# Performance work log

Measured on AMD Instinct MI355X. Metric: run time of the kernel, lower is better.

The kernel has to match this reference:

```python
import jax, jax.numpy as jnp
import numpy as np

B, D, K = 4096, 768, 60


def setup_inputs() -> dict:
    key = jax.random.key(0)
    k1, k2, k3 = jax.random.split(key, 3)
    user_emb = jax.random.normal(k1, (B, D), dtype=jnp.float32)
    pos_item_emb = jax.random.normal(k2, (B, D), dtype=jnp.float32)
    # Per-row negative indices into the in-batch item table, excluding the
    # row's own positive (emulates the exclusion/sampling done on host in torch).
    r = jax.random.randint(k3, (B, K), 0, B, dtype=jnp.int32)
    rows = jnp.arange(B, dtype=jnp.int32)[:, None]
    neg_indices = jnp.where(r == rows, (r + 1) % B, r)
    return {"user_emb": user_emb, "pos_item_emb": pos_item_emb,
            "neg_indices": neg_indices}


def reference(user_emb, pos_item_emb, neg_indices):
    # u2i contrastive loss: logits = [u.pos, u.neg_1..neg_K], label 0, mean CE.
    logits_pos = jnp.sum(user_emb * pos_item_emb, axis=-1)          # (B,)
    neg_embs = pos_item_emb[neg_indices]                            # (B, K, D)
    logits_neg = jnp.einsum('bd,bkd->bk', user_emb, neg_embs)      # (B, K)
    logits = jnp.concatenate([logits_pos[:, None], logits_neg], axis=1)
    loss = -jax.nn.log_softmax(logits, axis=-1)[:, 0]               # label = 0
    return jnp.mean(loss)
```

## Files before the change

kernel.cpp:

```cpp
#include <hip/hip_runtime.h>
#include <hip/hip_bf16.h>
#include <hip/hip_fp16.h>
#include <math.h>


#define NB 4096
#define ND 768
#define NK 60
#define ND4 (ND / 4)
#define NLOGITS (NK + 1)
#define NPAD 64

#define WS_LOGITS_OFF 0
#define WS_ITEMS_OFF  ((size_t)NB * NPAD * 4)
#define WS_LOSS_OFF   (WS_ITEMS_OFF + (size_t)NB * ND * 2)
#define WS_NEED       (WS_LOSS_OFF + (size_t)NB * 4)

typedef _Float16 h2 __attribute__((ext_vector_type(2)));
typedef float    f2 __attribute__((ext_vector_type(2)));

__global__ __launch_bounds__(256) void convert_items_f16(
    const float4* __restrict__ in, uint2* __restrict__ outh)
{
    int i = blockIdx.x * 256 + threadIdx.x;
    float4 v = in[i];
    h2 a = { (_Float16)v.x, (_Float16)v.y };
    h2 b = { (_Float16)v.z, (_Float16)v.w };
    uint2 r;
    r.x = __builtin_bit_cast(unsigned int, a);
    r.y = __builtin_bit_cast(unsigned int, b);
    outh[i] = r;
}

__global__ __launch_bounds__(256) void gather_dots(
    const float* __restrict__ user,
    const uint2* __restrict__ itemsh,
    const int* __restrict__ negidx,
    float* __restrict__ logits)
{
    const int tid  = threadIdx.x;
    const int lane = tid & 63;
    const int w    = blockIdx.x * 4 + (tid >> 6);
    const int b    = w >> 4;
    const int slot = w & 15;

    const float4* u4 = (const float4*)user + (size_t)b * ND4;
    float4 u0 = u4[lane];
    float4 u1 = u4[64 + lane];
    float4 u2 = u4[128 + lane];

    const int* nrow = negidx + (size_t)b * NK;
    const uint2* p[4];
    #pragma unroll
    for (int i = 0; i < 4; ++i) {
        int k = slot * 4 + i;
        int row = (k == 0 || k > NK) ? b : nrow[k - 1];
        p[i] = itemsh + (size_t)row * ND4;
    }

    uint2 v0[4], v1[4], v2[4];
    #pragma unroll
    for (int i = 0; i < 4; ++i) {
        v0[i] = p[i][lane];
        v1[i] = p[i][64 + lane];
        v2[i] = p[i][128 + lane];
    }

    float acc[4];
    #pragma unroll
    for (int i = 0; i < 4; ++i) {
        f2 a0 = __builtin_convertvector(__builtin_bit_cast(h2, v0[i].x), f2);
        f2 a1 = __builtin_convertvector(__builtin_bit_cast(h2, v0[i].y), f2);
        f2 b0 = __builtin_convertvector(__builtin_bit_cast(h2, v1[i].x), f2);
        f2 b1 = __builtin_convertvector(__builtin_bit_cast(h2, v1[i].y), f2);
        f2 c0 = __builtin_convertvector(__builtin_bit_cast(h2, v2[i].x), f2);
        f2 c1 = __builtin_convertvector(__builtin_bit_cast(h2, v2[i].y), f2);
        float a;
        a  = u0.x * a0.x + u0.y * a0.y + u0.z * a1.x + u0.w * a1.y;
        a += u1.x * b0.x + u1.y * b0.y + u1.z * b1.x + u1.w * b1.y;
        a += u2.x * c0.x + u2.y * c0.y + u2.z * c1.x + u2.w * c1.y;
        acc[i] = a;
    }

    #pragma unroll
    for (int off = 32; off > 0; off >>= 1) {
        #pragma unroll
        for (int i = 0; i < 4; ++i)
            acc[i] += __shfl_down(acc[i], off, 64);
    }

    if (lane == 0) {
        float4 st = { acc[0], acc[1], acc[2], acc[3] };
        ((float4*)logits)[(size_t)b * 16 + slot] = st;
    }
}

__global__ __launch_bounds__(256) void lse_loss(
    const float* __restrict__ logits, float* __restrict__ loss)
{
    const int tid  = threadIdx.x;
    const int lane = tid & 63;
    const int b    = blockIdx.x * 4 + (tid >> 6);

    float v  = (lane < NLOGITS) ? logits[(size_t)b * NPAD + lane] : -INFINITY;
    float p0 = __shfl(v, 0, 64);
    float m = v;
    #pragma unroll
    for (int off = 32; off > 0; off >>= 1)
        m = fmaxf(m, __shfl_down(m, off, 64));
    m = __shfl(m, 0, 64);
    float e = (lane < NLOGITS) ? __expf(v - m) : 0.0f;
    #pragma unroll
    for (int off = 32; off > 0; off >>= 1)
        e += __shfl_down(e, off, 64);
    if (lane == 0)
        loss[b] = m + __logf(e) - p0;
}

__global__ __launch_bounds__(256) void final_reduce(
    const float* __restrict__ loss, float* __restrict__ out)
{
    const int tid = threadIdx.x;
    const float4* l4 = (const float4*)loss;
    float s = 0.0f;
    #pragma unroll
    for (int j = 0; j < 4; ++j) {
        float4 v = l4[tid + 256 * j];
        s += v.x + v.y + v.z + v.w;
    }
    #pragma unroll
    for (int off = 32; off > 0; off >>= 1)
        s += __shfl_down(s, off, 64);
    __shared__ float ps[4];
    if ((tid & 63) == 0) ps[tid >> 6] = s;
    __syncthreads();
    if (tid == 0)
        out[0] = (ps[0] + ps[1] + ps[2] + ps[3]) * (1.0f / (float)NB);
}

__global__ __launch_bounds__(256) void u2i_loss_f32(
    const float* __restrict__ user,
    const float* __restrict__ items,
    const int* __restrict__ negidx,
    float* __restrict__ out)
{
    const int b    = blockIdx.x;
    const int tid  = threadIdx.x;
    const int wave = tid >> 6;
    const int lane = tid & 63;

    __shared__ int   rows_s[NPAD];
    __shared__ float logits[NPAD];

    if (tid < NPAD) {
        const int* nrow = negidx + (size_t)b * NK;
        rows_s[tid] = (tid == 0 || tid > NK) ? b : nrow[tid - 1];
    }
    const float4* u4 = (const float4*)user + (size_t)b * ND4;
    float4 u0 = u4[lane];
    float4 u1 = u4[64 + lane];
    float4 u2 = u4[128 + lane];
    __syncthreads();

    const float4* it4 = (const float4*)items;
    #pragma unroll
    for (int j = 0; j < 4; ++j) {
        int ks[4];
        const float4* p[4];
        #pragma unroll
        for (int i = 0; i < 4; ++i) {
            ks[i] = wave + j * 16 + i * 4;
            p[i]  = it4 + (size_t)rows_s[ks[i]] * ND4;
        }
        float4 v0[4], v1[4], v2[4];
        #pragma unroll
        for (int i = 0; i < 4; ++i) {
            v0[i] = p[i][lane];
            v1[i] = p[i][64 + lane];
            v2[i] = p[i][128 + lane];
        }
        float acc[4];
        #pragma unroll
        for (int i = 0; i < 4; ++i) {
            float a;
            a  = u0.x * v0[i].x + u0.y * v0[i].y + u0.z * v0[i].z + u0.w * v0[i].w;
            a += u1.x * v1[i].x + u1.y * v1[i].y + u1.z * v1[i].z + u1.w * v1[i].w;
            a += u2.x * v2[i].x + u2.y * v2[i].y + u2.z * v2[i].z + u2.w * v2[i].w;
            acc[i] = a;
        }
        #pragma unroll
        for (int off = 32; off > 0; off >>= 1) {
            #pragma unroll
            for (int i = 0; i < 4; ++i)
                acc[i] += __shfl_down(acc[i], off, 64);
        }
        if (lane == 0) {
            #pragma unroll
            for (int i = 0; i < 4; ++i)
                logits[ks[i]] = acc[i];
        }
    }
    __syncthreads();

    if (tid < 64) {
        float v = (tid < NLOGITS) ? logits[tid] : -INFINITY;
        float m = v;
        #pragma unroll
        for (int off = 32; off > 0; off >>= 1)
            m = fmaxf(m, __shfl_down(m, off, 64));
        m = __shfl(m, 0, 64);
        float e = (tid < NLOGITS) ? __expf(v - m) : 0.0f;
        #pragma unroll
        for (int off = 32; off > 0; off >>= 1)
            e += __shfl_down(e, off, 64);
        if (tid == 0) {
            float loss = m + __logf(e) - logits[0];
            atomicAdd(out, loss * (1.0f / (float)NB));
        }
    }
}

extern "C" void kernel_launch(void* const* d_in, const int* in_sizes, int n_in,
                              void* d_out, int out_size, void* d_ws, size_t ws_size,
                              hipStream_t stream) {
    const float* user  = (const float*)d_in[0];
    const float* items = (const float*)d_in[1];
    const int*   negi  = (const int*)d_in[2];
    float* out = (float*)d_out;

    if (ws_size >= WS_NEED) {
        char* ws = (char*)d_ws;
        float* logits = (float*)(ws + WS_LOGITS_OFF);
        uint2* itemsh = (uint2*)(ws + WS_ITEMS_OFF);
        float* loss   = (float*)(ws + WS_LOSS_OFF);

        convert_items_f16<<<(NB * ND / 4) / 256, 256, 0, stream>>>(
            (const float4*)items, itemsh);
        gather_dots<<<NB * 16 / 4, 256, 0, stream>>>(user, itemsh, negi, logits);
        lse_loss<<<NB / 4, 256, 0, stream>>>(logits, loss);
        final_reduce<<<1, 256, 0, stream>>>(loss, out);
    } else {
        hipMemsetAsync(out, 0, sizeof(float), stream);
        u2i_loss_f32<<<NB, 256, 0, stream>>>(user, items, negi, out);
    }
}
```

Baseline: 108.6 us.

## Convert user embeddings to fp16, use fdot2, and compute 8 logits per wave

```diff
diff --git a/kernel.cpp b/kernel.cpp
--- a/kernel.cpp
+++ b/kernel.cpp
@@ -7,91 +7,110 @@
 #define NB 4096
 #define ND 768
 #define NK 60
-#define ND4 (ND / 4)
+#define ND4  (ND / 4)
+#define NDU  (ND / 2)
 #define NLOGITS (NK + 1)
 #define NPAD 64
 
 #define WS_LOGITS_OFF 0
 #define WS_ITEMS_OFF  ((size_t)NB * NPAD * 4)
-#define WS_LOSS_OFF   (WS_ITEMS_OFF + (size_t)NB * ND * 2)
+#define WS_USER_OFF   (WS_ITEMS_OFF + (size_t)NB * ND * 2)
+#define WS_LOSS_OFF   (WS_USER_OFF + (size_t)NB * ND * 2)
 #define WS_NEED       (WS_LOSS_OFF + (size_t)NB * 4)
 
 typedef _Float16 h2 __attribute__((ext_vector_type(2)));
 typedef float    f2 __attribute__((ext_vector_type(2)));
 
-__global__ __launch_bounds__(256) void convert_items_f16(
-    const float4* __restrict__ in, uint2* __restrict__ outh)
+__device__ __forceinline__ float dot2_acc(unsigned int u, unsigned int v, float c) {
+#if __has_builtin(__builtin_amdgcn_fdot2)
+    return __builtin_amdgcn_fdot2(__builtin_bit_cast(h2, u),
+                                  __builtin_bit_cast(h2, v), c, false);
+#else
+    f2 a = __builtin_convertvector(__builtin_bit_cast(h2, u), f2);
+    f2 b = __builtin_convertvector(__builtin_bit_cast(h2, v), f2);
+    return c + a.x * b.x + a.y * b.y;
+#endif
+}
+
+__global__ __launch_bounds__(256) void convert_f16(
+    const float4* __restrict__ user, const float4* __restrict__ items,
+    uint2* __restrict__ userh, uint2* __restrict__ itemsh)
 {
     int i = blockIdx.x * 256 + threadIdx.x;
-    float4 v = in[i];
-    h2 a = { (_Float16)v.x, (_Float16)v.y };
-    h2 b = { (_Float16)v.z, (_Float16)v.w };
-    uint2 r;
-    r.x = __builtin_bit_cast(unsigned int, a);
-    r.y = __builtin_bit_cast(unsigned int, b);
-    outh[i] = r;
+    float4 u = user[i];
+    float4 v = items[i];
+    h2 ua = { (_Float16)u.x, (_Float16)u.y };
+    h2 ub = { (_Float16)u.z, (_Float16)u.w };
+    h2 va = { (_Float16)v.x, (_Float16)v.y };
+    h2 vb = { (_Float16)v.z, (_Float16)v.w };
+    uint2 ru, rv;
+    ru.x = __builtin_bit_cast(unsigned int, ua);
+    ru.y = __builtin_bit_cast(unsigned int, ub);
+    rv.x = __builtin_bit_cast(unsigned int, va);
+    rv.y = __builtin_bit_cast(unsigned int, vb);
+    userh[i]  = ru;
+    itemsh[i] = rv;
 }
 
 __global__ __launch_bounds__(256) void gather_dots(
-    const float* __restrict__ user,
-    const uint2* __restrict__ itemsh,
+    const unsigned int* __restrict__ userh,
+    const unsigned int* __restrict__ itemsh,
     const int* __restrict__ negidx,
     float* __restrict__ logits)
 {
     const int tid  = threadIdx.x;
     const int lane = tid & 63;
     const int w    = blockIdx.x * 4 + (tid >> 6);
-    const int b    = w >> 4;
-    const int slot = w & 15;
-
-    const float4* u4 = (const float4*)user + (size_t)b * ND4;
-    float4 u0 = u4[lane];
-    float4 u1 = u4[64 + lane];
-    float4 u2 = u4[128 + lane];
+    const int b    = w >> 3;
+    const int slot = w & 7;
 
     const int* nrow = negidx + (size_t)b * NK;
-    const uint2* p[4];
-    #pragma unroll
-    for (int i = 0; i < 4; ++i) {
-        int k = slot * 4 + i;
-        int row = (k == 0 || k > NK) ? b : nrow[k - 1];
-        p[i] = itemsh + (size_t)row * ND4;
-    }
-
-    uint2 v0[4], v1[4], v2[4];
-    #pragma unroll
-    for (int i = 0; i < 4; ++i) {
-        v0[i] = p[i][lane];
-        v1[i] = p[i][64 + lane];
-        v2[i] = p[i][128 + lane];
-    }
-
-    float acc[4];
-    #pragma unroll
-    for (int i = 0; i < 4; ++i) {
-        f2 a0 = __builtin_convertvector(__builtin_bit_cast(h2, v0[i].x), f2);
-        f2 a1 = __builtin_convertvector(__builtin_bit_cast(h2, v0[i].y), f2);
-        f2 b0 = __builtin_convertvector(__builtin_bit_cast(h2, v1[i].x), f2);
-        f2 b1 = __builtin_convertvector(__builtin_bit_cast(h2, v1[i].y), f2);
-        f2 c0 = __builtin_convertvector(__builtin_bit_cast(h2, v2[i].x), f2);
-        f2 c1 = __builtin_convertvector(__builtin_bit_cast(h2, v2[i].y), f2);
-        float a;
-        a  = u0.x * a0.x + u0.y * a0.y + u0.z * a1.x + u0.w * a1.y;
-        a += u1.x * b0.x + u1.y * b0.y + u1.z * b1.x + u1.w * b1.y;
-        a += u2.x * c0.x + u2.y * c0.y + u2.z * c1.x + u2.w * c1.y;
+    int rows[8];
+    #pragma unroll
+    for (int i = 0; i < 8; ++i) {
+        int k = slot * 8 + i;
+        rows[i] = (k == 0 || k > NK) ? b : nrow[k - 1];
+    }
+
+    const unsigned int* ur = userh + (size_t)b * NDU;
+    uint4 ua = ((const uint4*)ur)[lane];
+    uint2 ub = ((const uint2*)(ur + 256))[lane];
+
+    uint4 va[8];
+    uint2 vb[8];
+    #pragma unroll
+    for (int i = 0; i < 8; ++i) {
+        const unsigned int* ir = itemsh + (size_t)rows[i] * NDU;
+        va[i] = ((const uint4*)ir)[lane];
+        vb[i] = ((const uint2*)(ir + 256))[lane];
+    }
+
+    float acc[8];
+    #pragma unroll
+    for (int i = 0; i < 8; ++i) {
+        float a = 0.0f;
+        a = dot2_acc(ua.x, va[i].x, a);
+        a = dot2_acc(ua.y, va[i].y, a);
+        a = dot2_acc(ua.z, va[i].z, a);
+        a = dot2_acc(ua.w, va[i].w, a);
+        a = dot2_acc(ub.x, vb[i].x, a);
+        a = dot2_acc(ub.y, vb[i].y, a);
         acc[i] = a;
     }
 
     #pragma unroll
     for (int off = 32; off > 0; off >>= 1) {
         #pragma unroll
-        for (int i = 0; i < 4; ++i)
+        for (int i = 0; i < 8; ++i)
             acc[i] += __shfl_down(acc[i], off, 64);
     }
 
     if (lane == 0) {
-        float4 st = { acc[0], acc[1], acc[2], acc[3] };
-        ((float4*)logits)[(size_t)b * 16 + slot] = st;
+        float4* dst = (float4*)(logits + (size_t)b * NPAD + slot * 8);
+        float4 s0 = { acc[0], acc[1], acc[2], acc[3] };
+        float4 s1 = { acc[4], acc[5], acc[6], acc[7] };
+        dst[0] = s0;
+        dst[1] = s1;
     }
 }
 
@@ -230,13 +249,15 @@
 
     if (ws_size >= WS_NEED) {
         char* ws = (char*)d_ws;
-        float* logits = (float*)(ws + WS_LOGITS_OFF);
-        uint2* itemsh = (uint2*)(ws + WS_ITEMS_OFF);
-        float* loss   = (float*)(ws + WS_LOSS_OFF);
-
-        convert_items_f16<<<(NB * ND / 4) / 256, 256, 0, stream>>>(
-            (const float4*)items, itemsh);
-        gather_dots<<<NB * 16 / 4, 256, 0, stream>>>(user, itemsh, negi, logits);
+        float*        logits = (float*)(ws + WS_LOGITS_OFF);
+        uint2*        itemsh = (uint2*)(ws + WS_ITEMS_OFF);
+        uint2*        userh  = (uint2*)(ws + WS_USER_OFF);
+        float*        loss   = (float*)(ws + WS_LOSS_OFF);
+
+        convert_f16<<<(NB * ND / 4) / 256, 256, 0, stream>>>(
+            (const float4*)user, (const float4*)items, userh, itemsh);
+        gather_dots<<<NB * 8 / 4, 256, 0, stream>>>(
+            (const unsigned int*)userh, (const unsigned int*)itemsh, negi, logits);
         lse_loss<<<NB / 4, 256, 0, stream>>>(logits, loss);
         final_reduce<<<1, 256, 0, stream>>>(loss, out);
     } else {
```

After: 103.3 us. 4.8% less time.
